# Kernel optimization log

Measured on AMD Instinct MI355X. Metric: run time of the kernel, lower is better.

The kernel has to match this reference:

```python
import jax, jax.numpy as jnp
import numpy as np

BN_EPS = 1e-5

def setup_inputs() -> dict:
    key = jax.random.key(0)
    k1, k2, k3 = jax.random.split(key, 3)
    B, D_IN, D_OUT = 16384, 2048, 1024
    stdv = np.sqrt(1.5 / (D_IN + D_OUT))
    x = jax.random.normal(k1, (B, D_IN), dtype=jnp.float32)
    weight = jax.random.uniform(k2, (D_OUT, D_IN), dtype=jnp.float32, minval=-stdv, maxval=stdv)
    bias = jax.random.normal(k3, (D_OUT,), dtype=jnp.float32) * 0.01
    gamma = jnp.ones((D_OUT,), dtype=jnp.float32)
    beta = jnp.zeros((D_OUT,), dtype=jnp.float32)
    return {"x": x, "weight": weight, "bias": bias, "gamma": gamma, "beta": beta}

def reference(x, weight, bias, gamma, beta):
    # STE-binarized weights: forward uses sign(w) (>=0 -> +1), grad flows via clamp(w,-1,1)
    w_sign = jnp.where(weight >= 0, 1.0, -1.0).astype(weight.dtype)
    w_clip = jnp.clip(weight, -1.0, 1.0)
    w_bin = jax.lax.stop_gradient(w_sign - w_clip) + w_clip
    # y = x @ w_bin.T + bias   -> [B, D_OUT]
    y = jnp.einsum('bi,oi->bo', x, w_bin) + bias[None, :]
    # BatchNorm1d (training mode: batch statistics, biased variance)
    mean = jnp.mean(y, axis=0)
    var = jnp.mean((y - mean) ** 2, axis=0)
    y_norm = (y - mean) * jax.lax.rsqrt(var + BN_EPS)
    return y_norm * gamma + beta
```

## Files before the change

### kernel.cpp

```cpp
#include <hip/hip_runtime.h>
#include <hip/hip_bf16.h>

typedef __attribute__((ext_vector_type(4))) float f32x4;
typedef __attribute__((ext_vector_type(8))) __bf16 bf16x8;
typedef __attribute__((ext_vector_type(4))) unsigned int uint4v;

constexpr int M = 16384;
constexpr int N = 1024;
constexpr int K = 2048;
constexpr int BM = 256, BN = 256, BK = 32;
constexpr int NK = K / BK;
constexpr float BN_EPS = 1e-5f;
constexpr int TM2 = M / BM;

#define GLOAD_LDS16(g, l)                                                      \
  __builtin_amdgcn_global_load_lds(                                            \
      (const __attribute__((address_space(1))) void*)(g),                      \
      (__attribute__((address_space(3))) void*)(l), 16, 0, 0)

#define SB0 __builtin_amdgcn_sched_barrier(0)

__device__ __forceinline__ unsigned sgnbf(float f) {
  return (f >= 0.f) ? 0x3F80u : 0xBF80u;
}
__global__ __launch_bounds__(256) void binw_kernel(
    const float* __restrict__ w, uint4v* __restrict__ wb) {
  size_t i = (size_t)blockIdx.x * 256 + threadIdx.x;
  const f32x4* win = (const f32x4*)w;
  f32x4 v0 = win[i * 2];
  f32x4 v1 = win[i * 2 + 1];
  uint4v o;
  o.x = sgnbf(v0[0]) | (sgnbf(v0[1]) << 16);
  o.y = sgnbf(v0[2]) | (sgnbf(v0[3]) << 16);
  o.z = sgnbf(v1[0]) | (sgnbf(v1[1]) << 16);
  o.w = sgnbf(v1[2]) | (sgnbf(v1[3]) << 16);
  wb[i] = o;
}

__global__ __launch_bounds__(1024) void gemm_bin_kernel(
    const float* __restrict__ Af, const unsigned short* __restrict__ B,
    float* __restrict__ Y, float* __restrict__ psum, float* __restrict__ psq) {
  __shared__ unsigned short As[3][BM * BK];
  __shared__ unsigned short Bs[3][BN * BK];
  __shared__ float redsum[4][BN];
  __shared__ float redsq[4][BN];

  const int tid = threadIdx.x;
  const int wid = tid >> 6;
  const int lane = tid & 63;
  const int wr = wid >> 2, wc = wid & 3;

  const int bid = blockIdx.x;
  const int swz = (bid & 7) * 32 + (bid >> 3);
  const int tm = swz >> 2, tn = swz & 3;
  const size_t m0 = (size_t)tm * BM, n0 = (size_t)tn * BN;

  const int frow = lane & 15;
  const int fcb = lane >> 4;
  const int swzc = fcb ^ ((frow >> 1) & 3);
  const int aoff = (wr * 64 + frow) * BK + swzc * 8;
  const int boff = (wc * 64 + frow) * BK + swzc * 8;

  f32x4 acc[4][4];
#pragma unroll
  for (int m = 0; m < 4; ++m)
#pragma unroll
    for (int n = 0; n < 4; ++n)
#pragma unroll
      for (int j = 0; j < 4; ++j) acc[m][n][j] = 0.f;

  const int r0s = tid >> 2;
  const int c0s = (tid & 3) ^ ((r0s >> 1) & 3);
  const unsigned short* pB = B + (n0 + r0s) * (size_t)K + c0s * 8;

  const int rA0 = tid >> 2;
  const int cA = (tid & 3) ^ ((rA0 >> 1) & 3);
  const float* pAf = Af + (m0 + rA0) * (size_t)K + cA * 8;
  const int awb0 = rA0 * 32 + (tid & 3) * 8;
  f32x4 As_[2];

#define A_ISSUE(ktv)                                                           \
  {                                                                            \
    const size_t k0_ = (size_t)(ktv)*BK;                                       \
    As_[0] = *(const f32x4*)(pAf + k0_);                                       \
    As_[1] = *(const f32x4*)(pAf + k0_ + 4);                                   \
  }
#define B_ISSUE(ss, ktv)                                                       \
  { GLOAD_LDS16(pB + (size_t)(ktv)*BK, &Bs[ss][wid * 512]); }
#define A_WRITE(ss)                                                            \
  {                                                                            \
    bf16x8 v0_;                                                                \
    _Pragma("unroll") for (int j_ = 0; j_ < 4; ++j_) {                         \
      v0_[j_] = (__bf16)As_[0][j_];                                            \
      v0_[4 + j_] = (__bf16)As_[1][j_];                                        \
    }                                                                          \
    *(bf16x8*)&As[ss][awb0] = v0_;                                             \
  }

#define WAITL                                                                  \
  asm volatile("s_waitcnt lgkmcnt(0)" ::: "memory");                           \
  __builtin_amdgcn_sched_barrier(0);

#define LDA(s, m) (*(const bf16x8*)&As[s][aoff + (m)*512])
#define LDB(s, n) (*(const bf16x8*)&Bs[s][boff + (n)*512])

#define MF(mi, av)                                                             \
  _Pragma("unroll") for (int n = 0; n < 4; ++n) acc[mi][n] =                   \
      __builtin_amdgcn_mfma_f32_16x16x32_bf16(av, b_[n], acc[mi][n], 0, 0, 0);

#define WINDOW(s, ktv, MODE)                                                   \
  {                                                                            \
    bf16x8 b_[4], a0, a1, a2, a3;                                              \
    if (MODE == 0) {                                                           \
      A_ISSUE((ktv) + 2);         \
      SB0;                                                                     \
    }                                                                          \
    b_[0] = LDB(s, 0);                                                         \
    b_[1] = LDB(s, 1);                                                         \
    b_[2] = LDB(s, 2);                                                         \
    b_[3] = LDB(s, 3);                                                         \
    a0 = LDA(s, 0);                                                            \
    a1 = LDA(s, 1);                                                            \
    if (MODE == 0) {                                                           \
      B_ISSUE(((ktv) + 2) % 3, (ktv) + 2);           \
      SB0;                                                                     \
    }                                                                          \
    WAITL                                                                      \
    __builtin_amdgcn_s_setprio(1);                                             \
    a2 = LDA(s, 2);                                                            \
    a3 = LDA(s, 3);                                                            \
    MF(0, a0)                                                                  \
    MF(1, a1)                                                                  \
    __builtin_amdgcn_s_setprio(0);                                             \
    WAITL                                                                      \
    __builtin_amdgcn_s_setprio(1);                                             \
    MF(2, a2)                                                                  \
    MF(3, a3)                                                                  \
    __builtin_amdgcn_s_setprio(0);                                             \
    SB0;                                                                       \
    if (MODE == 0) {                                                           \
      asm volatile("s_waitcnt vmcnt(1)" ::: "memory");                         \
      A_WRITE(((ktv) + 2) % 3);                                                \
    } else if (MODE == 1) {                                                    \
      asm volatile("s_waitcnt vmcnt(0)" ::: "memory");                         \
    }                                                                          \
    if (MODE != 2) {                                                           \
      asm volatile("s_waitcnt lgkmcnt(0)" ::: "memory");                       \
      __builtin_amdgcn_s_barrier();                                            \
      asm volatile("" ::: "memory");                                           \
    }                                                                          \
  }

  A_ISSUE(0);
  SB0;
  B_ISSUE(0, 0);
  SB0;
  asm volatile("s_waitcnt vmcnt(1)" ::: "memory");
  A_WRITE(0);
  A_ISSUE(1);
  SB0;
  B_ISSUE(1, 1);
  SB0;
  asm volatile("s_waitcnt vmcnt(1)" ::: "memory");
  A_WRITE(1);
  asm volatile("s_waitcnt lgkmcnt(0)" ::: "memory");
  __builtin_amdgcn_s_barrier();
  asm volatile("" ::: "memory");

  for (int kt = 0; kt < NK - 4; kt += 3) {
    WINDOW(0, kt, 0);
    WINDOW(1, kt + 1, 0);
    WINDOW(2, kt + 2, 0);
  }
  WINDOW(0, NK - 4, 0);
  WINDOW(1, NK - 3, 0);
  WINDOW(2, NK - 2, 1);
  WINDOW(0, NK - 1, 2);

#pragma unroll
  for (int m = 0; m < 4; ++m) {
    const size_t r0 = m0 + wr * 64 + m * 16 + fcb * 4;
#pragma unroll
    for (int n = 0; n < 4; ++n) {
      const size_t c = n0 + wc * 64 + n * 16 + frow;
#pragma unroll
      for (int j = 0; j < 4; ++j) Y[(r0 + j) * N + c] = acc[m][n][j];
    }
  }

  float cs[4], cq[4];
#pragma unroll
  for (int n = 0; n < 4; ++n) {
    float s = 0.f, q = 0.f;
#pragma unroll
    for (int m = 0; m < 4; ++m)
#pragma unroll
      for (int j = 0; j < 4; ++j) {
        float v = acc[m][n][j];
        s += v;
        q += v * v;
      }
    cs[n] = s;
    cq[n] = q;
  }
#pragma unroll
  for (int n = 0; n < 4; ++n) {
    cs[n] += __shfl_xor(cs[n], 16);
    cs[n] += __shfl_xor(cs[n], 32);
    cq[n] += __shfl_xor(cq[n], 16);
    cq[n] += __shfl_xor(cq[n], 32);
  }
  __syncthreads();
  if (fcb == 0) {
#pragma unroll
    for (int n = 0; n < 4; ++n) {
      redsum[wr][wc * 64 + n * 16 + frow] = cs[n];
      redsq[wr][wc * 64 + n * 16 + frow] = cq[n];
    }
  }
  __syncthreads();
  if (tid < BN) {
    const size_t c = n0 + tid;
    psum[(size_t)tm * N + c] =
        redsum[0][tid] + redsum[1][tid] + redsum[2][tid] + redsum[3][tid];
    psq[(size_t)tm * N + c] =
        redsq[0][tid] + redsq[1][tid] + redsq[2][tid] + redsq[3][tid];
  }
}

__global__ __launch_bounds__(256) void bnstats_kernel(
    const float* __restrict__ psum, const float* __restrict__ psq,
    const float* __restrict__ gamma, const float* __restrict__ beta,
    float* __restrict__ scale, float* __restrict__ shift) {
  const int c = blockIdx.x * 256 + threadIdx.x;
  float s = 0.f, q = 0.f;
  for (int i = 0; i < TM2; ++i) {
    s += psum[i * N + c];
    q += psq[i * N + c];
  }
  const float mean = s * (1.f / (float)M);
  const float var = q * (1.f / (float)M) - mean * mean;
  const float inv = rsqrtf(var + BN_EPS);
  const float sc = gamma[c] * inv;
  scale[c] = sc;
  shift[c] = beta[c] - mean * sc;
}

__global__ __launch_bounds__(256) void bnapply_kernel(
    float* __restrict__ Y, const float* __restrict__ scale,
    const float* __restrict__ shift) {
  const size_t i = (size_t)blockIdx.x * 256 + threadIdx.x;
  f32x4 y = ((const f32x4*)Y)[i];
  const int c = (int)((i * 4) & (N - 1));
  f32x4 sc = *(const f32x4*)&scale[c];
  f32x4 sh = *(const f32x4*)&shift[c];
  ((f32x4*)Y)[i] = y * sc + sh;
}

extern "C" void kernel_launch(void* const* d_in, const int* in_sizes, int n_in,
                              void* d_out, int out_size, void* d_ws,
                              size_t ws_size, hipStream_t stream) {
  const float* x = (const float*)d_in[0];
  const float* w = (const float*)d_in[1];
  const float* gamma = (const float*)d_in[3];
  const float* beta = (const float*)d_in[4];
  float* Y = (float*)d_out;

  char* ws = (char*)d_ws;
  uint4v* wb = (uint4v*)ws;
  float* psum = (float*)(ws + (size_t)N * K * 2);
  float* psq = psum + (size_t)TM2 * N;
  float* scale = psq + (size_t)TM2 * N;
  float* shift = scale + N;

  binw_kernel<<<(N * K / 8) / 256, 256, 0, stream>>>(w, wb);
  gemm_bin_kernel<<<(M / BM) * (N / BN), 1024, 0, stream>>>(
      x, (const unsigned short*)wb, Y, psum, psq);
  bnstats_kernel<<<N / 256, 256, 0, stream>>>(psum, psq, gamma, beta, scale,
                                              shift);
  bnapply_kernel<<<(M * N / 4) / 256, 256, 0, stream>>>(Y, scale, shift);
}
```

Measured before the change: 106.6 us.

## Fuse BN stats and apply into GEMM via cooperative grid sync

Launches the GEMM cooperatively (256 blocks of 1024 threads) and adds a grid-wide sync after the per-tile partial sums are written. Each block then reduces the column statistics for its own 256 columns, computes scale and shift, and writes the normalized output straight from its accumulators. This removes the unnormalized Y write, the read-modify-write pass over the 64 MB output, and two kernel launches. In exchange it requires all blocks to be co-resident, and every block waits at the grid barrier while holding its accumulators in registers.

```diff
diff --git a/kernel.cpp b/kernel.cpp
--- a/kernel.cpp
+++ b/kernel.cpp
@@ -1,5 +1,8 @@
 #include <hip/hip_runtime.h>
 #include <hip/hip_bf16.h>
+#include <hip/hip_cooperative_groups.h>
+
+namespace cg = cooperative_groups;
 
 typedef __attribute__((ext_vector_type(4))) float f32x4;
 typedef __attribute__((ext_vector_type(8))) __bf16 bf16x8;
@@ -39,7 +42,8 @@
 
 __global__ __launch_bounds__(1024) void gemm_bin_kernel(
     const float* __restrict__ Af, const unsigned short* __restrict__ B,
-    float* __restrict__ Y, float* __restrict__ psum, float* __restrict__ psq) {
+    float* __restrict__ Y, float* __restrict__ psum, float* __restrict__ psq,
+    const float* __restrict__ gamma, const float* __restrict__ beta) {
   __shared__ unsigned short As[3][BM * BK];
   __shared__ unsigned short Bs[3][BN * BK];
   __shared__ float redsum[4][BN];
@@ -177,17 +181,6 @@
   WINDOW(2, NK - 2, 1);
   WINDOW(0, NK - 1, 2);
 
-#pragma unroll
-  for (int m = 0; m < 4; ++m) {
-    const size_t r0 = m0 + wr * 64 + m * 16 + fcb * 4;
-#pragma unroll
-    for (int n = 0; n < 4; ++n) {
-      const size_t c = n0 + wc * 64 + n * 16 + frow;
-#pragma unroll
-      for (int j = 0; j < 4; ++j) Y[(r0 + j) * N + c] = acc[m][n][j];
-    }
-  }
-
   float cs[4], cq[4];
 #pragma unroll
   for (int n = 0; n < 4; ++n) {
@@ -226,35 +219,51 @@
     psq[(size_t)tm * N + c] =
         redsq[0][tid] + redsq[1][tid] + redsq[2][tid] + redsq[3][tid];
   }
-}
-
-__global__ __launch_bounds__(256) void bnstats_kernel(
-    const float* __restrict__ psum, const float* __restrict__ psq,
-    const float* __restrict__ gamma, const float* __restrict__ beta,
-    float* __restrict__ scale, float* __restrict__ shift) {
-  const int c = blockIdx.x * 256 + threadIdx.x;
-  float s = 0.f, q = 0.f;
-  for (int i = 0; i < TM2; ++i) {
-    s += psum[i * N + c];
-    q += psq[i * N + c];
-  }
-  const float mean = s * (1.f / (float)M);
-  const float var = q * (1.f / (float)M) - mean * mean;
-  const float inv = rsqrtf(var + BN_EPS);
-  const float sc = gamma[c] * inv;
-  scale[c] = sc;
-  shift[c] = beta[c] - mean * sc;
-}
-
-__global__ __launch_bounds__(256) void bnapply_kernel(
-    float* __restrict__ Y, const float* __restrict__ scale,
-    const float* __restrict__ shift) {
-  const size_t i = (size_t)blockIdx.x * 256 + threadIdx.x;
-  f32x4 y = ((const f32x4*)Y)[i];
-  const int c = (int)((i * 4) & (N - 1));
-  f32x4 sc = *(const f32x4*)&scale[c];
-  f32x4 sh = *(const f32x4*)&shift[c];
-  ((f32x4*)Y)[i] = y * sc + sh;
+
+  __threadfence();
+  cg::this_grid().sync();
+  __threadfence();
+
+  const int cl = tid & 255;
+  const int qd = tid >> 8;
+  {
+    float s = 0.f, q = 0.f;
+    const float* ps = psum + n0 + cl;
+    const float* pq = psq + n0 + cl;
+    for (int i = qd * 16; i < qd * 16 + 16; ++i) {
+      s += ps[(size_t)i * N];
+      q += pq[(size_t)i * N];
+    }
+    redsum[qd][cl] = s;
+    redsq[qd][cl] = q;
+  }
+  __syncthreads();
+  if (tid < 256) {
+    const float S =
+        redsum[0][cl] + redsum[1][cl] + redsum[2][cl] + redsum[3][cl];
+    const float Q = redsq[0][cl] + redsq[1][cl] + redsq[2][cl] + redsq[3][cl];
+    const float mean = S * (1.f / (float)M);
+    const float var = Q * (1.f / (float)M) - mean * mean;
+    const float inv = rsqrtf(var + BN_EPS);
+    const float sc = gamma[n0 + cl] * inv;
+    redsum[0][cl] = sc;
+    redsq[0][cl] = beta[n0 + cl] - mean * sc;
+  }
+  __syncthreads();
+
+#pragma unroll
+  for (int m = 0; m < 4; ++m) {
+    const size_t r0 = m0 + wr * 64 + m * 16 + fcb * 4;
+#pragma unroll
+    for (int n = 0; n < 4; ++n) {
+      const int cloc = wc * 64 + n * 16 + frow;
+      const float sc = redsum[0][cloc];
+      const float sh = redsq[0][cloc];
+      float* yp = Y + r0 * N + n0 + cloc;
+#pragma unroll
+      for (int j = 0; j < 4; ++j) yp[(size_t)j * N] = acc[m][n][j] * sc + sh;
+    }
+  }
 }
 
 extern "C" void kernel_launch(void* const* d_in, const int* in_sizes, int n_in,
@@ -270,13 +279,13 @@
   uint4v* wb = (uint4v*)ws;
   float* psum = (float*)(ws + (size_t)N * K * 2);
   float* psq = psum + (size_t)TM2 * N;
-  float* scale = psq + (size_t)TM2 * N;
-  float* shift = scale + N;
 
   binw_kernel<<<(N * K / 8) / 256, 256, 0, stream>>>(w, wb);
-  gemm_bin_kernel<<<(M / BM) * (N / BN), 1024, 0, stream>>>(
-      x, (const unsigned short*)wb, Y, psum, psq);
-  bnstats_kernel<<<N / 256, 256, 0, stream>>>(psum, psq, gamma, beta, scale,
-                                              shift);
-  bnapply_kernel<<<(M * N / 4) / 256, 256, 0, stream>>>(Y, scale, shift);
-}
+
+  const unsigned short* Bp = (const unsigned short*)wb;
+  void* args[] = {(void*)&x,    (void*)&Bp,    (void*)&Y,   (void*)&psum,
+                  (void*)&psq,  (void*)&gamma, (void*)&beta};
+  hipLaunchCooperativeKernel(reinterpret_cast<void*>(gemm_bin_kernel),
+                             dim3((M / BM) * (N / BN)), dim3(1024), args, 0,
+                             stream);
+}
```

Result: slower. 259.6 us (+143.6%).

## Load A fragments directly to registers and restructure GEMM warp tiling

Applied to the files above, without the earlier changes.

The GEMM kernel now runs 512 threads (two blocks per CU requested) instead of 1024. Each wave owns 32 rows by all 256 columns, and its A fragments are loaded from global fp32 straight into registers and converted to bf16, so A is no longer staged through LDS. B is staged in a double-buffered LDS tile with BK=64 via direct global-to-LDS loads, which halves the number of barriers. In exchange there are far more accumulator registers (128 floats per lane), A reuse drops, and each wave reads all 16 B fragments per k-step.

```diff
diff --git a/kernel.cpp b/kernel.cpp
--- a/kernel.cpp
+++ b/kernel.cpp
@@ -8,8 +8,8 @@
 constexpr int M = 16384;
 constexpr int N = 1024;
 constexpr int K = 2048;
-constexpr int BM = 256, BN = 256, BK = 32;
-constexpr int NK = K / BK;
+constexpr int BM = 256, BN = 256;
+constexpr int NK2 = K / 64;
 constexpr float BN_EPS = 1e-5f;
 constexpr int TM2 = M / BM;
 
@@ -19,6 +19,9 @@
       (__attribute__((address_space(3))) void*)(l), 16, 0, 0)
 
 #define SB0 __builtin_amdgcn_sched_barrier(0)
+#define BARRIER __builtin_amdgcn_s_barrier()
+#define VMC(n) asm volatile("s_waitcnt vmcnt(" #n ")" ::: "memory")
+#define LGKM0 asm volatile("s_waitcnt lgkmcnt(0)" ::: "memory")
 
 __device__ __forceinline__ unsigned sgnbf(float f) {
   return (f >= 0.f) ? 0x3F80u : 0xBF80u;
@@ -37,18 +40,16 @@
   wb[i] = o;
 }
 
-__global__ __launch_bounds__(1024) void gemm_bin_kernel(
+__global__ __launch_bounds__(512, 2) void gemm_bin_kernel(
     const float* __restrict__ Af, const unsigned short* __restrict__ B,
     float* __restrict__ Y, float* __restrict__ psum, float* __restrict__ psq) {
-  __shared__ unsigned short As[3][BM * BK];
-  __shared__ unsigned short Bs[3][BN * BK];
-  __shared__ float redsum[4][BN];
-  __shared__ float redsq[4][BN];
+  __shared__ unsigned short Bs[2][16384];
+  __shared__ float redsum[8][256];
+  __shared__ float redsq[8][256];
 
   const int tid = threadIdx.x;
   const int wid = tid >> 6;
   const int lane = tid & 63;
-  const int wr = wid >> 2, wc = wid & 3;
 
   const int bid = blockIdx.x;
   const int swz = (bid & 7) * 32 + (bid >> 3);
@@ -57,174 +58,153 @@
 
   const int frow = lane & 15;
   const int fcb = lane >> 4;
-  const int swzc = fcb ^ ((frow >> 1) & 3);
-  const int aoff = (wr * 64 + frow) * BK + swzc * 8;
-  const int boff = (wc * 64 + frow) * BK + swzc * 8;
-
-  f32x4 acc[4][4];
-#pragma unroll
-  for (int m = 0; m < 4; ++m)
-#pragma unroll
-    for (int n = 0; n < 4; ++n)
-#pragma unroll
-      for (int j = 0; j < 4; ++j) acc[m][n][j] = 0.f;
-
-  const int r0s = tid >> 2;
-  const int c0s = (tid & 3) ^ ((r0s >> 1) & 3);
-  const unsigned short* pB = B + (n0 + r0s) * (size_t)K + c0s * 8;
-
-  const int rA0 = tid >> 2;
-  const int cA = (tid & 3) ^ ((rA0 >> 1) & 3);
-  const float* pAf = Af + (m0 + rA0) * (size_t)K + cA * 8;
-  const int awb0 = rA0 * 32 + (tid & 3) * 8;
-  f32x4 As_[2];
-
-#define A_ISSUE(ktv)                                                           \
-  {                                                                            \
-    const size_t k0_ = (size_t)(ktv)*BK;                                       \
-    As_[0] = *(const f32x4*)(pAf + k0_);                                       \
-    As_[1] = *(const f32x4*)(pAf + k0_ + 4);                                   \
-  }
-#define B_ISSUE(ss, ktv)                                                       \
-  { GLOAD_LDS16(pB + (size_t)(ktv)*BK, &Bs[ss][wid * 512]); }
-#define A_WRITE(ss)                                                            \
-  {                                                                            \
-    bf16x8 v0_;                                                                \
+  const int bbase = frow * 32 + ((fcb ^ ((frow >> 1) & 3)) * 8);
+
+  const float* pA = Af + (m0 + wid * 32 + frow) * (size_t)K + fcb * 8;
+
+  const int gc = (lane & 3) ^ ((lane >> 3) & 3);
+  const unsigned short* pBg =
+      B + (n0 + wid * 16 + (lane >> 2)) * (size_t)K + gc * 8;
+
+  f32x4 acc[2][16];
+#pragma unroll
+  for (int mi = 0; mi < 2; ++mi)
+#pragma unroll
+    for (int nj = 0; nj < 16; ++nj)
+#pragma unroll
+      for (int j = 0; j < 4; ++j) acc[mi][nj][j] = 0.f;
+
+  f32x4 xr0, xr1, xr2, xr3, xr4, xr5, xr6, xr7;
+
+#define AL(ktv)                                                                \
+  {                                                                            \
+    const float* p0_ = pA + (size_t)(ktv)*64;                                  \
+    const float* p1_ = pA + 16 * (size_t)K + (size_t)(ktv)*64;                 \
+    xr0 = *(const f32x4*)(p0_);                                   \
+    xr1 = *(const f32x4*)(p0_ + 4);                                            \
+    xr2 = *(const f32x4*)(p0_ + 32);                              \
+    xr3 = *(const f32x4*)(p0_ + 36);                                           \
+    xr4 = *(const f32x4*)(p1_);                                   \
+    xr5 = *(const f32x4*)(p1_ + 4);                                            \
+    xr6 = *(const f32x4*)(p1_ + 32);                              \
+    xr7 = *(const f32x4*)(p1_ + 36);                                           \
+  }
+
+#define CVT1(dst, ra, rb)                                                      \
+  {                                                                            \
+    bf16x8 v_;                                                                 \
     _Pragma("unroll") for (int j_ = 0; j_ < 4; ++j_) {                         \
-      v0_[j_] = (__bf16)As_[0][j_];                                            \
-      v0_[4 + j_] = (__bf16)As_[1][j_];                                        \
-    }                                                                          \
-    *(bf16x8*)&As[ss][awb0] = v0_;                                             \
-  }
-
-#define WAITL                                                                  \
-  asm volatile("s_waitcnt lgkmcnt(0)" ::: "memory");                           \
-  __builtin_amdgcn_sched_barrier(0);
-
-#define LDA(s, m) (*(const bf16x8*)&As[s][aoff + (m)*512])
-#define LDB(s, n) (*(const bf16x8*)&Bs[s][boff + (n)*512])
-
-#define MF(mi, av)                                                             \
-  _Pragma("unroll") for (int n = 0; n < 4; ++n) acc[mi][n] =                   \
-      __builtin_amdgcn_mfma_f32_16x16x32_bf16(av, b_[n], acc[mi][n], 0, 0, 0);
-
-#define WINDOW(s, ktv, MODE)                                                   \
-  {                                                                            \
-    bf16x8 b_[4], a0, a1, a2, a3;                                              \
-    if (MODE == 0) {                                                           \
-      A_ISSUE((ktv) + 2);         \
-      SB0;                                                                     \
-    }                                                                          \
-    b_[0] = LDB(s, 0);                                                         \
-    b_[1] = LDB(s, 1);                                                         \
-    b_[2] = LDB(s, 2);                                                         \
-    b_[3] = LDB(s, 3);                                                         \
-    a0 = LDA(s, 0);                                                            \
-    a1 = LDA(s, 1);                                                            \
-    if (MODE == 0) {                                                           \
-      B_ISSUE(((ktv) + 2) % 3, (ktv) + 2);           \
-      SB0;                                                                     \
-    }                                                                          \
-    WAITL                                                                      \
+      v_[j_] = (__bf16)(ra)[j_];                                               \
+      v_[4 + j_] = (__bf16)(rb)[j_];                                           \
+    }                                                                          \
+    dst = v_;                                                                  \
+  }
+
+#define BG(rd, ktv, NS)                                                        \
+  GLOAD_LDS16(                                                                 \
+      pBg + (size_t)((rd)&1) * 128 * K + (size_t)(ktv)*64 + ((rd) >> 1) * 32,  \
+      &Bs[NS][((rd) >> 1) * 8192 + (((rd)&1) * 128 + wid * 16) * 32])
+
+#define PHASE(S, ks, njh, aA, aB)                                              \
+  {                                                                            \
+    bf16x8 b_[8];                                                              \
+    _Pragma("unroll") for (int j_ = 0; j_ < 8; ++j_) b_[j_] =                  \
+        *(const bf16x8*)&Bs[S][(ks)*8192 + ((njh)*8 + j_) * 512 + bbase];      \
     __builtin_amdgcn_s_setprio(1);                                             \
-    a2 = LDA(s, 2);                                                            \
-    a3 = LDA(s, 3);                                                            \
-    MF(0, a0)                                                                  \
-    MF(1, a1)                                                                  \
-    __builtin_amdgcn_s_setprio(0);                                             \
-    WAITL                                                                      \
-    __builtin_amdgcn_s_setprio(1);                                             \
-    MF(2, a2)                                                                  \
-    MF(3, a3)                                                                  \
+    _Pragma("unroll") for (int j_ = 0; j_ < 8; ++j_) {                         \
+      acc[0][(njh)*8 + j_] = __builtin_amdgcn_mfma_f32_16x16x32_bf16(          \
+          aA, b_[j_], acc[0][(njh)*8 + j_], 0, 0, 0);                          \
+      acc[1][(njh)*8 + j_] = __builtin_amdgcn_mfma_f32_16x16x32_bf16(          \
+          aB, b_[j_], acc[1][(njh)*8 + j_], 0, 0, 0);                          \
+    }                                                                          \
     __builtin_amdgcn_s_setprio(0);                                             \
     SB0;                                                                       \
-    if (MODE == 0) {                                                           \
-      asm volatile("s_waitcnt vmcnt(1)" ::: "memory");                         \
-      A_WRITE(((ktv) + 2) % 3);                                                \
-    } else if (MODE == 1) {                                                    \
-      asm volatile("s_waitcnt vmcnt(0)" ::: "memory");                         \
-    }                                                                          \
-    if (MODE != 2) {                                                           \
-      asm volatile("s_waitcnt lgkmcnt(0)" ::: "memory");                       \
-      __builtin_amdgcn_s_barrier();                                            \
-      asm volatile("" ::: "memory");                                           \
-    }                                                                          \
-  }
-
-  A_ISSUE(0);
+  }
+
+#define ITER(S, NS, ktv, STG)                                                  \
+  {                                                                            \
+    bf16x8 a00, a01, a10, a11;                                                 \
+    CVT1(a00, xr0, xr1);                                                       \
+    CVT1(a01, xr2, xr3);                                                       \
+    CVT1(a10, xr4, xr5);                                                       \
+    CVT1(a11, xr6, xr7);                                                       \
+    SB0;                                                                       \
+    if (STG) {                                                                 \
+      BG(0, (ktv) + 1, NS);                                                    \
+      BG(1, (ktv) + 1, NS);                                                    \
+      BG(2, (ktv) + 1, NS);                                                    \
+      BG(3, (ktv) + 1, NS);                                                    \
+      AL((ktv) + 1);                                                           \
+      SB0;                                                                     \
+    }                                                                          \
+    PHASE(S, 0, 0, a00, a10);                                                  \
+    PHASE(S, 0, 1, a00, a10);                                                  \
+    PHASE(S, 1, 0, a01, a11);                                                  \
+    PHASE(S, 1, 1, a01, a11);                                                  \
+    if (STG) {                                                                 \
+      LGKM0;                                                                   \
+      VMC(8);                                                                  \
+      BARRIER;                                                                 \
+    }                                                                          \
+  }
+
+  BG(0, 0, 0);
+  BG(1, 0, 0);
+  BG(2, 0, 0);
+  BG(3, 0, 0);
+  AL(0);
   SB0;
-  B_ISSUE(0, 0);
-  SB0;
-  asm volatile("s_waitcnt vmcnt(1)" ::: "memory");
-  A_WRITE(0);
-  A_ISSUE(1);
-  SB0;
-  B_ISSUE(1, 1);
-  SB0;
-  asm volatile("s_waitcnt vmcnt(1)" ::: "memory");
-  A_WRITE(1);
-  asm volatile("s_waitcnt lgkmcnt(0)" ::: "memory");
-  __builtin_amdgcn_s_barrier();
-  asm volatile("" ::: "memory");
-
-  for (int kt = 0; kt < NK - 4; kt += 3) {
-    WINDOW(0, kt, 0);
-    WINDOW(1, kt + 1, 0);
-    WINDOW(2, kt + 2, 0);
-  }
-  WINDOW(0, NK - 4, 0);
-  WINDOW(1, NK - 3, 0);
-  WINDOW(2, NK - 2, 1);
-  WINDOW(0, NK - 1, 2);
-
-#pragma unroll
-  for (int m = 0; m < 4; ++m) {
-    const size_t r0 = m0 + wr * 64 + m * 16 + fcb * 4;
-#pragma unroll
-    for (int n = 0; n < 4; ++n) {
-      const size_t c = n0 + wc * 64 + n * 16 + frow;
-#pragma unroll
-      for (int j = 0; j < 4; ++j) Y[(r0 + j) * N + c] = acc[m][n][j];
-    }
-  }
-
-  float cs[4], cq[4];
-#pragma unroll
-  for (int n = 0; n < 4; ++n) {
+  VMC(8);
+  BARRIER;
+
+  for (int kt = 0; kt < NK2 - 2; kt += 2) {
+    ITER(0, 1, kt, 1);
+    ITER(1, 0, kt + 1, 1);
+  }
+  ITER(0, 1, NK2 - 2, 1);
+  ITER(1, 0, NK2 - 1, 0);
+
+#pragma unroll
+  for (int nj = 0; nj < 16; ++nj) {
     float s = 0.f, q = 0.f;
 #pragma unroll
-    for (int m = 0; m < 4; ++m)
+    for (int mi = 0; mi < 2; ++mi)
 #pragma unroll
       for (int j = 0; j < 4; ++j) {
-        float v = acc[m][n][j];
+        float v = acc[mi][nj][j];
         s += v;
         q += v * v;
       }
-    cs[n] = s;
-    cq[n] = q;
-  }
-#pragma unroll
-  for (int n = 0; n < 4; ++n) {
-    cs[n] += __shfl_xor(cs[n], 16);
-    cs[n] += __shfl_xor(cs[n], 32);
-    cq[n] += __shfl_xor(cq[n], 16);
-    cq[n] += __shfl_xor(cq[n], 32);
-  }
-  __syncthreads();
-  if (fcb == 0) {
-#pragma unroll
-    for (int n = 0; n < 4; ++n) {
-      redsum[wr][wc * 64 + n * 16 + frow] = cs[n];
-      redsq[wr][wc * 64 + n * 16 + frow] = cq[n];
+    s += __shfl_xor(s, 16);
+    s += __shfl_xor(s, 32);
+    q += __shfl_xor(q, 16);
+    q += __shfl_xor(q, 32);
+    if (fcb == 0) {
+      redsum[wid][nj * 16 + frow] = s;
+      redsq[wid][nj * 16 + frow] = q;
     }
   }
   __syncthreads();
   if (tid < BN) {
-    const size_t c = n0 + tid;
-    psum[(size_t)tm * N + c] =
-        redsum[0][tid] + redsum[1][tid] + redsum[2][tid] + redsum[3][tid];
-    psq[(size_t)tm * N + c] =
-        redsq[0][tid] + redsq[1][tid] + redsq[2][tid] + redsq[3][tid];
+    float s = 0.f, q = 0.f;
+#pragma unroll
+    for (int w = 0; w < 8; ++w) {
+      s += redsum[w][tid];
+      q += redsq[w][tid];
+    }
+    psum[(size_t)tm * N + n0 + tid] = s;
+    psq[(size_t)tm * N + n0 + tid] = q;
+  }
+
+#pragma unroll
+  for (int mi = 0; mi < 2; ++mi) {
+    const size_t r0 = m0 + wid * 32 + mi * 16 + fcb * 4;
+#pragma unroll
+    for (int nj = 0; nj < 16; ++nj) {
+      float* yp = Y + r0 * N + n0 + nj * 16 + frow;
+#pragma unroll
+      for (int j = 0; j < 4; ++j) yp[(size_t)j * N] = acc[mi][nj][j];
+    }
   }
 }
 
@@ -274,7 +254,7 @@
   float* shift = scale + N;
 
   binw_kernel<<<(N * K / 8) / 256, 256, 0, stream>>>(w, wb);
-  gemm_bin_kernel<<<(M / BM) * (N / BN), 1024, 0, stream>>>(
+  gemm_bin_kernel<<<(M / BM) * (N / BN), 512, 0, stream>>>(
       x, (const unsigned short*)wb, Y, psum, psq);
   bnstats_kernel<<<N / 256, 256, 0, stream>>>(psum, psq, gamma, beta, scale,
                                               shift);
```

Result: slower. 131.9 us (+23.7%).
